# Kernel optimization log

Measured on AMD Instinct MI355X. Metric: run time of the kernel, lower is better.

## Reference

```python
import jax, jax.numpy as jnp
import numpy as np

D_IN = 1024
D_EMB = 512
HIDDEN = 256
NUM_CLASSES = 64
N_SUPPORT = 4096
N_QUERY = 8192


def setup_inputs() -> dict:
    key = jax.random.key(0)
    ks = jax.random.split(key, 8)
    scale_e = 1.0 / np.sqrt(D_IN)
    scale_1 = 1.0 / np.sqrt(2 * D_EMB)
    scale_2 = 1.0 / np.sqrt(HIDDEN)
    return {
        "support_data": jax.random.normal(ks[0], (N_SUPPORT, D_IN), jnp.float32),
        "query_data": jax.random.normal(ks[1], (N_QUERY, D_IN), jnp.float32),
        "support_label": jax.random.randint(ks[2], (N_SUPPORT,), 0, NUM_CLASSES, jnp.int32),
        "W_e": jax.random.normal(ks[3], (D_IN, D_EMB), jnp.float32) * scale_e,
        "b_e": jnp.zeros((D_EMB,), jnp.float32),
        "W1": jax.random.normal(ks[4], (2 * D_EMB, HIDDEN), jnp.float32) * scale_1,
        "b1": jnp.zeros((HIDDEN,), jnp.float32),
        "W2": jax.random.normal(ks[5], (HIDDEN, 1), jnp.float32) * scale_2,
        "b2": jnp.zeros((1,), jnp.float32),
    }


def reference(support_data, query_data, support_label, W_e, b_e, W1, b1, W2, b2):
    # embedding_net: Linear + ReLU
    s_emb = jax.nn.relu(support_data @ W_e + b_e)  # [Ns, D_EMB]
    q_emb = jax.nn.relu(query_data @ W_e + b_e)    # [Nq, D_EMB]

    # per-class mean of support embeddings (segment mean; labels are 0..C-1,
    # matching torch.unique()'s sorted order)
    sums = jax.ops.segment_sum(s_emb, support_label, num_segments=NUM_CLASSES)
    counts = jax.ops.segment_sum(jnp.ones((s_emb.shape[0],), s_emb.dtype),
                                 support_label, num_segments=NUM_CLASSES)
    means = sums / jnp.maximum(counts, 1.0)[:, None]  # [C, D_EMB]

    # relation_net on concat(query, class_mean): split first linear so the
    # [Nq*C, 2*D_EMB] concat is never materialized (same math).
    Wq, Wc = W1[:D_EMB], W1[D_EMB:]
    h = jax.nn.relu(q_emb @ Wq[:, None, :].squeeze(1) @ jnp.eye(HIDDEN, dtype=W1.dtype)
                    if False else
                    (q_emb @ Wq)[:, None, :] + (means @ Wc)[None, :, :] + b1)  # [Nq, C, HIDDEN]
    scores = jax.nn.sigmoid(h @ W2 + b2)  # [Nq, C, 1]
    # torch version stacks [1,1]-shaped scores -> [Nq, C, 1, 1]
    return scores[:, :, None, :]
```

## Files before the change

### kernel.cpp

```cpp
#include <hip/hip_runtime.h>
#include <hip/hip_bf16.h>

#define D_IN 1024
#define D_EMB 512
#define HIDDEN 256
#define NUM_CLASSES 64
#define N_SUPPORT 4096
#define N_QUERY 8192

typedef __bf16 bf16x8 __attribute__((ext_vector_type(8)));
typedef __bf16 bf16x4 __attribute__((ext_vector_type(4)));
typedef float f32x4 __attribute__((ext_vector_type(4)));

#define GLOAD_LDS16(g, l)                                                          \
  __builtin_amdgcn_global_load_lds(                                                \
      (const __attribute__((address_space(1))) unsigned int*)(g),                  \
      (__attribute__((address_space(3))) unsigned int*)(l), 16, 0, 0)

__global__ void transpose_weights(const float* __restrict__ W_e,
                                  const float* __restrict__ W1,
                                  __bf16* __restrict__ WeT,
                                  __bf16* __restrict__ WqT) {
  __shared__ float tile[32][33];
  const float* in;
  __bf16* out;
  int bx, by, rows, cols;
  int b = blockIdx.x;
  if (b < 512) {
    in = W_e; out = WeT; rows = D_IN; cols = D_EMB;
    bx = (b & 15) * 32; by = (b >> 4) * 32;
  } else {
    b -= 512;
    in = W1; out = WqT; rows = D_EMB; cols = HIDDEN;
    bx = (b & 7) * 32; by = (b >> 3) * 32;
  }
  int tx = threadIdx.x;
  int ty = threadIdx.y;
#pragma unroll
  for (int i = ty; i < 32; i += 8)
    tile[i][tx] = in[(long)(by + i) * cols + bx + tx];
  __syncthreads();
#pragma unroll
  for (int i = ty; i < 32; i += 8)
    out[(long)(bx + i) * rows + by + tx] = (__bf16)tile[tx][i];
}

__global__ __launch_bounds__(256, 2) void gemm_emb(
    const float* __restrict__ support, const float* __restrict__ query,
    const __bf16* __restrict__ BT, const float* __restrict__ bias,
    __bf16* __restrict__ C) {
  constexpr int BM = 128, BN = 128, BK = 32;
  constexpr int N = D_EMB, K = D_IN;
  constexpr int LDA_S = 40;
  constexpr int WN = BN / 2, NR = WN / 16, MR = 4;

  __shared__ __align__(16) __bf16 As[BM * LDA_S];
  __shared__ __align__(16) __bf16 Bs[BN * BK];

  const int tid = threadIdx.x;
  const int wave = tid >> 6;
  const int lane = tid & 63;
  const int m0 = blockIdx.x * BM;
  const int n0 = blockIdx.y * BN;
  const int wr = wave >> 1;
  const int wc = wave & 1;
  const int l16 = lane & 15;
  const int half = lane >> 4;

  const float* Abase =
      (m0 < N_SUPPORT) ? (support + (long)m0 * K) : (query + (long)(m0 - N_SUPPORT) * K);

  f32x4 acc[MR][NR];
#pragma unroll
  for (int m = 0; m < MR; ++m)
#pragma unroll
    for (int n = 0; n < NR; ++n) acc[m][n] = (f32x4)0.0f;

  for (int k0 = 0; k0 < K; k0 += BK) {
    float4 av[4];
#pragma unroll
    for (int q = 0; q < 4; ++q) {
      int idx = q * 256 + tid;
      int row = idx >> 3;
      int c4 = idx & 7;
      av[q] = *(const float4*)(Abase + (long)row * K + k0 + c4 * 4);
    }
#pragma unroll
    for (int q = 0; q < 2; ++q) {
      int chunk = q * 256 + tid;
      int row = chunk >> 2;
      int kc = chunk & 3;
      GLOAD_LDS16(BT + (long)(n0 + row) * K + k0 + kc * 8, Bs + chunk * 8);
    }
#pragma unroll
    for (int q = 0; q < 4; ++q) {
      int idx = q * 256 + tid;
      int row = idx >> 3;
      int c4 = idx & 7;
      bf16x4 o;
      o[0] = (__bf16)av[q].x; o[1] = (__bf16)av[q].y;
      o[2] = (__bf16)av[q].z; o[3] = (__bf16)av[q].w;
      *(bf16x4*)(As + row * LDA_S + c4 * 4) = o;
    }
    asm volatile("s_waitcnt vmcnt(0)" ::: "memory");
    __syncthreads();

    bf16x8 a[MR], b[NR];
#pragma unroll
    for (int m = 0; m < MR; ++m)
      a[m] = *(const bf16x8*)(As + (wr * 64 + m * 16 + l16) * LDA_S + half * 8);
#pragma unroll
    for (int n = 0; n < NR; ++n)
      b[n] = *(const bf16x8*)(Bs + (wc * WN + n * 16 + l16) * BK + half * 8);
#pragma unroll
    for (int m = 0; m < MR; ++m)
#pragma unroll
      for (int n = 0; n < NR; ++n)
        acc[m][n] = __builtin_amdgcn_mfma_f32_16x16x32_bf16(a[m], b[n],
                                                            acc[m][n], 0, 0, 0);
    __syncthreads();
  }

#pragma unroll
  for (int m = 0; m < MR; ++m)
#pragma unroll
    for (int n = 0; n < NR; ++n)
#pragma unroll
      for (int j = 0; j < 4; ++j) {
        int row = m0 + wr * 64 + m * 16 + half * 4 + j;
        int col = n0 + wc * WN + n * 16 + l16;
        float v = fmaxf(acc[m][n][j] + bias[col], 0.0f);
        C[(long)row * N + col] = (__bf16)v;
      }
}

__global__ __launch_bounds__(256, 2) void gemm_qp(
    const __bf16* __restrict__ A, const __bf16* __restrict__ BT,
    const float* __restrict__ bias, float* __restrict__ C, int M, int N, int K) {
  constexpr int BM = 128, BN = 64, BK = 32;
  constexpr int WN = BN / 2, NR = WN / 16, MR = 4;

  __shared__ __align__(16) __bf16 As[BM * BK];
  __shared__ __align__(16) __bf16 Bs[BN * BK];

  const int tid = threadIdx.x;
  const int wave = tid >> 6;
  const int lane = tid & 63;
  const int m0 = blockIdx.x * BM;
  const int n0 = blockIdx.y * BN;
  const int wr = wave >> 1;
  const int wc = wave & 1;
  const int l16 = lane & 15;
  const int half = lane >> 4;

  f32x4 acc[MR][NR];
#pragma unroll
  for (int m = 0; m < MR; ++m)
#pragma unroll
    for (int n = 0; n < NR; ++n) acc[m][n] = (f32x4)0.0f;

  for (int k0 = 0; k0 < K; k0 += BK) {
#pragma unroll
    for (int q = 0; q < BM / 64; ++q) {
      int chunk = q * 256 + tid;
      int row = chunk >> 2;
      int kc = chunk & 3;
      GLOAD_LDS16(A + (long)(m0 + row) * K + k0 + kc * 8, As + chunk * 8);
    }
    {
      int chunk = tid;
      int row = chunk >> 2;
      int kc = chunk & 3;
      GLOAD_LDS16(BT + (long)(n0 + row) * K + k0 + kc * 8, Bs + chunk * 8);
    }
    asm volatile("s_waitcnt vmcnt(0)" ::: "memory");
    __syncthreads();

    bf16x8 a[MR], b[NR];
#pragma unroll
    for (int m = 0; m < MR; ++m)
      a[m] = *(const bf16x8*)(As + (wr * 64 + m * 16 + l16) * BK + half * 8);
#pragma unroll
    for (int n = 0; n < NR; ++n)
      b[n] = *(const bf16x8*)(Bs + (wc * WN + n * 16 + l16) * BK + half * 8);
#pragma unroll
    for (int m = 0; m < MR; ++m)
#pragma unroll
      for (int n = 0; n < NR; ++n)
        acc[m][n] = __builtin_amdgcn_mfma_f32_16x16x32_bf16(a[m], b[n],
                                                            acc[m][n], 0, 0, 0);
    __syncthreads();
  }

#pragma unroll
  for (int m = 0; m < MR; ++m)
#pragma unroll
    for (int n = 0; n < NR; ++n)
#pragma unroll
      for (int j = 0; j < 4; ++j) {
        int row = m0 + wr * 64 + m * 16 + half * 4 + j;
        int col = n0 + wc * WN + n * 16 + l16;
        C[(long)row * N + col] = acc[m][n][j] + bias[col];
      }
}

__global__ __launch_bounds__(256) void proto_partial(
    const __bf16* __restrict__ s_emb, const int* __restrict__ labels,
    float* __restrict__ sums_part, int* __restrict__ cnt_part) {
  const int c = blockIdx.x;
  const int s = blockIdx.y;
  const int tid = threadIdx.x;
  const int j0 = s * (N_SUPPORT / 8);
  float a0 = 0.0f, a1 = 0.0f;
  int count = 0;
#pragma unroll 4
  for (int j = j0; j < j0 + N_SUPPORT / 8; j += 4) {
    int4 lab4 = *(const int4*)(labels + j);
#pragma unroll
    for (int u = 0; u < 4; ++u) {
      int lab = (u == 0) ? lab4.x : (u == 1) ? lab4.y : (u == 2) ? lab4.z : lab4.w;
      if (lab == c) {
        const __bf16* r = s_emb + (long)(j + u) * D_EMB;
        a0 += (float)r[tid];
        a1 += (float)r[tid + 256];
        ++count;
      }
    }
  }
  float* dst = sums_part + (long)(c * 8 + s) * D_EMB;
  dst[tid] = a0;
  dst[tid + 256] = a1;
  if (tid == 0) cnt_part[c * 8 + s] = count;
}

__global__ __launch_bounds__(256) void proto_cpb(
    const float* __restrict__ sums_part, const int* __restrict__ cnt_part,
    const float* __restrict__ W1, float* __restrict__ cpb_part) {
  __shared__ float ls[128];
  const int c = blockIdx.x;
  const int kc = blockIdx.y;
  const int k0 = kc * 128;
  const int tid = threadIdx.x;

  int nc = 0;
#pragma unroll
  for (int s = 0; s < 8; ++s) nc += cnt_part[c * 8 + s];
  float inv = 1.0f / fmaxf((float)nc, 1.0f);

  if (tid < 128) {
    float v = 0.0f;
#pragma unroll
    for (int s = 0; s < 8; ++s)
      v += sums_part[(long)(c * 8 + s) * D_EMB + k0 + tid];
    ls[tid] = v * inv;
  }
  __syncthreads();

  float acc = 0.0f;
#pragma unroll 8
  for (int k = 0; k < 128; ++k)
    acc = fmaf(ls[k], W1[(long)(D_EMB + k0 + k) * HIDDEN + tid], acc);
  cpb_part[((long)kc * NUM_CLASSES + c) * HIDDEN + tid] = acc;
}

__global__ void cpb_reduce(const float* __restrict__ cpb_part,
                           float* __restrict__ cpb) {
  int i = blockIdx.x * 256 + threadIdx.x;
  const int n = NUM_CLASSES * HIDDEN;
  cpb[i] = cpb_part[i] + cpb_part[n + i] + cpb_part[2 * n + i] +
           cpb_part[3 * n + i];
}

__global__ __launch_bounds__(256) void score_kernel(
    const float* __restrict__ qp, const float* __restrict__ cpb,
    const float* __restrict__ W2, const float* __restrict__ b2,
    float* __restrict__ out) {
  constexpr int CPB_S = 260;
  __shared__ __align__(16) float cpb_s[NUM_CLASSES * CPB_S];
  __shared__ __align__(16) float qp_s[32 * HIDDEN];
  __shared__ __align__(16) float w2_s[HIDDEN];

  const int tid = threadIdx.x;
  const int w = tid >> 6;
  const int c = tid & 63;
  const int qb0 = blockIdx.x * 32;

  w2_s[tid] = W2[tid];
  for (int i = tid; i < NUM_CLASSES * HIDDEN; i += 256)
    cpb_s[(i >> 8) * CPB_S + (i & (HIDDEN - 1))] = cpb[i];
  for (int i = tid; i < 32 * HIDDEN; i += 256)
    qp_s[i] = qp[(long)qb0 * HIDDEN + i];
  __syncthreads();

  const float bb = b2[0];
  float acc[8];
#pragma unroll
  for (int q = 0; q < 8; ++q) acc[q] = 0.0f;

  const float* crow = cpb_s + c * CPB_S;
  const float* qbase = qp_s + (w * 8) * HIDDEN;

#pragma unroll 4
  for (int kc = 0; kc < HIDDEN / 4; ++kc) {
    f32x4 cv = *(const f32x4*)(crow + kc * 4);
    f32x4 wv = *(const f32x4*)(w2_s + kc * 4);
#pragma unroll
    for (int q = 0; q < 8; ++q) {
      f32x4 qv = *(const f32x4*)(qbase + q * HIDDEN + kc * 4);
      acc[q] = fmaf(fmaxf(qv[0] + cv[0], 0.0f), wv[0], acc[q]);
      acc[q] = fmaf(fmaxf(qv[1] + cv[1], 0.0f), wv[1], acc[q]);
      acc[q] = fmaf(fmaxf(qv[2] + cv[2], 0.0f), wv[2], acc[q]);
      acc[q] = fmaf(fmaxf(qv[3] + cv[3], 0.0f), wv[3], acc[q]);
    }
  }

#pragma unroll
  for (int q = 0; q < 8; ++q) {
    float x = acc[q] + bb;
    out[(long)(qb0 + w * 8 + q) * NUM_CLASSES + c] = 1.0f / (1.0f + __expf(-x));
  }
}

extern "C" void kernel_launch(void* const* d_in, const int* in_sizes, int n_in,
                              void* d_out, int out_size, void* d_ws,
                              size_t ws_size, hipStream_t stream) {
  const float* support = (const float*)d_in[0];
  const float* query   = (const float*)d_in[1];
  const int*   labels  = (const int*)d_in[2];
  const float* W_e     = (const float*)d_in[3];
  const float* b_e     = (const float*)d_in[4];
  const float* W1      = (const float*)d_in[5];
  const float* b1      = (const float*)d_in[6];
  const float* W2      = (const float*)d_in[7];
  const float* b2      = (const float*)d_in[8];
  float* out = (float*)d_out;

  char* ws = (char*)d_ws;
  size_t off = 0;
  auto alloc = [&](size_t bytes) {
    void* p = ws + off;
    off = (off + bytes + 255) & ~(size_t)255;
    return p;
  };
  const long NTOT = N_SUPPORT + N_QUERY;
  __bf16* WeT = (__bf16*)alloc((size_t)D_EMB * D_IN * 2);
  __bf16* WqT = (__bf16*)alloc((size_t)HIDDEN * D_EMB * 2);
  __bf16* emb = (__bf16*)alloc((size_t)NTOT * D_EMB * 2);
  float*  qp  = (float*)alloc((size_t)N_QUERY * HIDDEN * 4);
  float*  sums_part = (float*)alloc((size_t)NUM_CLASSES * 8 * D_EMB * 4);
  int*    cnt_part  = (int*)alloc((size_t)NUM_CLASSES * 8 * 4);
  float*  cpb_part  = (float*)alloc((size_t)4 * NUM_CLASSES * HIDDEN * 4);
  float*  cpb       = (float*)alloc((size_t)NUM_CLASSES * HIDDEN * 4);

  transpose_weights<<<640, dim3(32, 8), 0, stream>>>(W_e, W1, WeT, WqT);

  gemm_emb<<<dim3(NTOT / 128, D_EMB / 128), 256, 0, stream>>>(
      support, query, WeT, b_e, emb);

  proto_partial<<<dim3(NUM_CLASSES, 8), 256, 0, stream>>>(emb, labels, sums_part,
                                                          cnt_part);
  proto_cpb<<<dim3(NUM_CLASSES, 4), 256, 0, stream>>>(sums_part, cnt_part, W1,
                                                      cpb_part);
  cpb_reduce<<<NUM_CLASSES * HIDDEN / 256, 256, 0, stream>>>(cpb_part, cpb);

  gemm_qp<<<dim3(N_QUERY / 128, HIDDEN / 64), 256, 0, stream>>>(
      emb + (long)N_SUPPORT * D_EMB, WqT, b1, qp, N_QUERY, HIDDEN, D_EMB);

  score_kernel<<<N_QUERY / 32, 256, 0, stream>>>(qp, cpb, W2, b2, out);
}
```

Baseline: 100.0 us.

## Double-buffer LDS in both GEMMs, shrink emb tile, add grouped block swizzle

Both GEMM kernels now use double-buffered shared memory, so the global loads for the next K-tile are issued before the MFMA work on the current tile and only one barrier is needed per iteration. gemm_emb shrinks its N tile from 128 to 64, which doubles the grid to 768 blocks. Both kernels switch to a 1D grid with a grouped mapping (8 M-tiles per group) to improve L2 reuse of the A rows. The costs are more LDS per block and higher register pressure from holding the A prefetch, and the smaller N tile means each fp32 A row is read and converted twice as often.

Result: no change. 101.1 us (+1.0%).

```diff
diff --git a/kernel.cpp b/kernel.cpp
--- a/kernel.cpp
+++ b/kernel.cpp
@@ -49,26 +49,34 @@
     const float* __restrict__ support, const float* __restrict__ query,
     const __bf16* __restrict__ BT, const float* __restrict__ bias,
     __bf16* __restrict__ C) {
-  constexpr int BM = 128, BN = 128, BK = 32;
+  constexpr int BM = 128, BN = 64, BK = 32;
   constexpr int N = D_EMB, K = D_IN;
   constexpr int LDA_S = 40;
-  constexpr int WN = BN / 2, NR = WN / 16, MR = 4;
-
-  __shared__ __align__(16) __bf16 As[BM * LDA_S];
-  __shared__ __align__(16) __bf16 Bs[BN * BK];
+  constexpr int NT = K / BK;
+  constexpr int MR = 4, NR = 2;
+
+  __shared__ __align__(16) __bf16 As[2][BM * LDA_S];
+  __shared__ __align__(16) __bf16 Bs[2][BN * BK];
 
   const int tid = threadIdx.x;
-  const int wave = tid >> 6;
-  const int lane = tid & 63;
-  const int m0 = blockIdx.x * BM;
-  const int n0 = blockIdx.y * BN;
-  const int wr = wave >> 1;
-  const int wc = wave & 1;
-  const int l16 = lane & 15;
-  const int half = lane >> 4;
-
-  const float* Abase =
-      (m0 < N_SUPPORT) ? (support + (long)m0 * K) : (query + (long)(m0 - N_SUPPORT) * K);
+  const int wave = tid >> 6, lane = tid & 63;
+  const int wr = wave >> 1, wc = wave & 1;
+  const int l16 = lane & 15, half = lane >> 4;
+
+  const int s = blockIdx.x;
+  const int m_t = (s & 7) + (s >> 6) * 8;
+  const int n_t = (s >> 3) & 7;
+  const int m0 = m_t * BM, n0 = n_t * BN;
+
+  const float* Abase = (m0 < N_SUPPORT)
+                           ? support + (long)m0 * K
+                           : query + (long)(m0 - N_SUPPORT) * K;
+
+  const int ar0 = tid >> 2, ar1 = (tid + 256) >> 2;
+  const int ac = tid & 3;
+  const int brow = tid >> 2, bkc = tid & 3;
+
+  float4 av[2][2];
 
   f32x4 acc[MR][NR];
 #pragma unroll
@@ -76,50 +84,70 @@
 #pragma unroll
     for (int n = 0; n < NR; ++n) acc[m][n] = (f32x4)0.0f;
 
-  for (int k0 = 0; k0 < K; k0 += BK) {
-    float4 av[4];
-#pragma unroll
-    for (int q = 0; q < 4; ++q) {
-      int idx = q * 256 + tid;
-      int row = idx >> 3;
-      int c4 = idx & 7;
-      av[q] = *(const float4*)(Abase + (long)row * K + k0 + c4 * 4);
-    }
-#pragma unroll
-    for (int q = 0; q < 2; ++q) {
-      int chunk = q * 256 + tid;
-      int row = chunk >> 2;
-      int kc = chunk & 3;
-      GLOAD_LDS16(BT + (long)(n0 + row) * K + k0 + kc * 8, Bs + chunk * 8);
-    }
-#pragma unroll
-    for (int q = 0; q < 4; ++q) {
-      int idx = q * 256 + tid;
-      int row = idx >> 3;
-      int c4 = idx & 7;
-      bf16x4 o;
-      o[0] = (__bf16)av[q].x; o[1] = (__bf16)av[q].y;
-      o[2] = (__bf16)av[q].z; o[3] = (__bf16)av[q].w;
-      *(bf16x4*)(As + row * LDA_S + c4 * 4) = o;
-    }
-    asm volatile("s_waitcnt vmcnt(0)" ::: "memory");
+#define LOAD_A(t)                                                         \
+  {                                                                       \
+    const float* p0 = Abase + (long)ar0 * K + (t) * BK + ac * 8;          \
+    const float* p1 = Abase + (long)ar1 * K + (t) * BK + ac * 8;          \
+    av[0][0] = *(const float4*)(p0);                                      \
+    av[0][1] = *(const float4*)(p0 + 4);                                  \
+    av[1][0] = *(const float4*)(p1);                                      \
+    av[1][1] = *(const float4*)(p1 + 4);                                  \
+  }
+
+#define WRITE_A(buf)                                                      \
+  {                                                                       \
+    bf16x8 o0, o1;                                                        \
+    o0[0] = (__bf16)av[0][0].x; o0[1] = (__bf16)av[0][0].y;               \
+    o0[2] = (__bf16)av[0][0].z; o0[3] = (__bf16)av[0][0].w;               \
+    o0[4] = (__bf16)av[0][1].x; o0[5] = (__bf16)av[0][1].y;               \
+    o0[6] = (__bf16)av[0][1].z; o0[7] = (__bf16)av[0][1].w;               \
+    o1[0] = (__bf16)av[1][0].x; o1[1] = (__bf16)av[1][0].y;               \
+    o1[2] = (__bf16)av[1][0].z; o1[3] = (__bf16)av[1][0].w;               \
+    o1[4] = (__bf16)av[1][1].x; o1[5] = (__bf16)av[1][1].y;               \
+    o1[6] = (__bf16)av[1][1].z; o1[7] = (__bf16)av[1][1].w;               \
+    *(bf16x8*)(&As[buf][ar0 * LDA_S + ac * 8]) = o0;                      \
+    *(bf16x8*)(&As[buf][ar1 * LDA_S + ac * 8]) = o1;                      \
+  }
+
+#define GLD_B(t, buf)                                                     \
+  GLOAD_LDS16(BT + (long)(n0 + brow) * K + (t) * BK + bkc * 8,            \
+              &Bs[buf][tid * 8]);
+
+#define COMPUTE(buf)                                                      \
+  {                                                                       \
+    bf16x8 a[MR], b[NR];                                                  \
+    _Pragma("unroll") for (int m = 0; m < MR; ++m)                        \
+        a[m] = *(const bf16x8*)(&As[buf][(wr * 64 + m * 16 + l16) *       \
+                                             LDA_S + half * 8]);          \
+    _Pragma("unroll") for (int n = 0; n < NR; ++n)                        \
+        b[n] = *(const bf16x8*)(&Bs[buf][(wc * 32 + n * 16 + l16) * BK +  \
+                                         half * 8]);                      \
+    _Pragma("unroll") for (int m = 0; m < MR; ++m)                        \
+        _Pragma("unroll") for (int n = 0; n < NR; ++n)                    \
+            acc[m][n] = __builtin_amdgcn_mfma_f32_16x16x32_bf16(          \
+                a[m], b[n], acc[m][n], 0, 0, 0);                          \
+  }
+
+  LOAD_A(0);
+  GLD_B(0, 0);
+  WRITE_A(0);
+  __syncthreads();
+
+  int cur = 0;
+  for (int t = 0; t < NT - 1; ++t) {
+    LOAD_A(t + 1);
+    GLD_B(t + 1, cur ^ 1);
+    COMPUTE(cur);
+    WRITE_A(cur ^ 1);
     __syncthreads();
-
-    bf16x8 a[MR], b[NR];
-#pragma unroll
-    for (int m = 0; m < MR; ++m)
-      a[m] = *(const bf16x8*)(As + (wr * 64 + m * 16 + l16) * LDA_S + half * 8);
-#pragma unroll
-    for (int n = 0; n < NR; ++n)
-      b[n] = *(const bf16x8*)(Bs + (wc * WN + n * 16 + l16) * BK + half * 8);
-#pragma unroll
-    for (int m = 0; m < MR; ++m)
-#pragma unroll
-      for (int n = 0; n < NR; ++n)
-        acc[m][n] = __builtin_amdgcn_mfma_f32_16x16x32_bf16(a[m], b[n],
-                                                            acc[m][n], 0, 0, 0);
-    __syncthreads();
-  }
+    cur ^= 1;
+  }
+  COMPUTE(cur);
+
+#undef LOAD_A
+#undef WRITE_A
+#undef GLD_B
+#undef COMPUTE
 
 #pragma unroll
   for (int m = 0; m < MR; ++m)
@@ -128,7 +156,7 @@
 #pragma unroll
       for (int j = 0; j < 4; ++j) {
         int row = m0 + wr * 64 + m * 16 + half * 4 + j;
-        int col = n0 + wc * WN + n * 16 + l16;
+        int col = n0 + wc * 32 + n * 16 + l16;
         float v = fmaxf(acc[m][n][j] + bias[col], 0.0f);
         C[(long)row * N + col] = (__bf16)v;
       }
@@ -136,22 +164,28 @@
 
 __global__ __launch_bounds__(256, 2) void gemm_qp(
     const __bf16* __restrict__ A, const __bf16* __restrict__ BT,
-    const float* __restrict__ bias, float* __restrict__ C, int M, int N, int K) {
+    const float* __restrict__ bias, float* __restrict__ C) {
   constexpr int BM = 128, BN = 64, BK = 32;
-  constexpr int WN = BN / 2, NR = WN / 16, MR = 4;
-
-  __shared__ __align__(16) __bf16 As[BM * BK];
-  __shared__ __align__(16) __bf16 Bs[BN * BK];
+  constexpr int N = HIDDEN, K = D_EMB;
+  constexpr int NT = K / BK;
+  constexpr int MR = 4, NR = 2;
+
+  __shared__ __align__(16) __bf16 As[2][BM * BK];
+  __shared__ __align__(16) __bf16 Bs[2][BN * BK];
 
   const int tid = threadIdx.x;
-  const int wave = tid >> 6;
-  const int lane = tid & 63;
-  const int m0 = blockIdx.x * BM;
-  const int n0 = blockIdx.y * BN;
-  const int wr = wave >> 1;
-  const int wc = wave & 1;
-  const int l16 = lane & 15;
-  const int half = lane >> 4;
+  const int wave = tid >> 6, lane = tid & 63;
+  const int wr = wave >> 1, wc = wave & 1;
+  const int l16 = lane & 15, half = lane >> 4;
+
+  const int s = blockIdx.x;
+  const int m_t = (s & 7) + (s >> 5) * 8;
+  const int n_t = (s >> 3) & 3;
+  const int m0 = m_t * BM, n0 = n_t * BN;
+
+  const int arow0 = tid >> 2, arow1 = (tid + 256) >> 2;
+  const int akc = tid & 3;
+  const int brow = tid >> 2, bkc = tid & 3;
 
   f32x4 acc[MR][NR];
 #pragma unroll
@@ -159,38 +193,45 @@
 #pragma unroll
     for (int n = 0; n < NR; ++n) acc[m][n] = (f32x4)0.0f;
 
-  for (int k0 = 0; k0 < K; k0 += BK) {
-#pragma unroll
-    for (int q = 0; q < BM / 64; ++q) {
-      int chunk = q * 256 + tid;
-      int row = chunk >> 2;
-      int kc = chunk & 3;
-      GLOAD_LDS16(A + (long)(m0 + row) * K + k0 + kc * 8, As + chunk * 8);
-    }
-    {
-      int chunk = tid;
-      int row = chunk >> 2;
-      int kc = chunk & 3;
-      GLOAD_LDS16(BT + (long)(n0 + row) * K + k0 + kc * 8, Bs + chunk * 8);
-    }
-    asm volatile("s_waitcnt vmcnt(0)" ::: "memory");
+#define STAGE(t, buf)                                                     \
+  {                                                                       \
+    GLOAD_LDS16(A + (long)(m0 + arow0) * K + (t) * BK + akc * 8,          \
+                &As[buf][tid * 8]);                                       \
+    GLOAD_LDS16(A + (long)(m0 + arow1) * K + (t) * BK + akc * 8,          \
+                &As[buf][(tid + 256) * 8]);                               \
+    GLOAD_LDS16(BT + (long)(n0 + brow) * K + (t) * BK + bkc * 8,          \
+                &Bs[buf][tid * 8]);                                       \
+  }
+
+#define COMPUTE(buf)                                                      \
+  {                                                                       \
+    bf16x8 a[MR], b[NR];                                                  \
+    _Pragma("unroll") for (int m = 0; m < MR; ++m)                        \
+        a[m] = *(const bf16x8*)(&As[buf][(wr * 64 + m * 16 + l16) * BK +  \
+                                         half * 8]);                      \
+    _Pragma("unroll") for (int n = 0; n < NR; ++n)                        \
+        b[n] = *(const bf16x8*)(&Bs[buf][(wc * 32 + n * 16 + l16) * BK +  \
+                                         half * 8]);                      \
+    _Pragma("unroll") for (int m = 0; m < MR; ++m)                        \
+        _Pragma("unroll") for (int n = 0; n < NR; ++n)                    \
+            acc[m][n] = __builtin_amdgcn_mfma_f32_16x16x32_bf16(          \
+                a[m], b[n], acc[m][n], 0, 0, 0);                          \
+  }
+
+  STAGE(0, 0);
+  __syncthreads();
+
+  int cur = 0;
+  for (int t = 0; t < NT - 1; ++t) {
+    STAGE(t + 1, cur ^ 1);
+    COMPUTE(cur);
     __syncthreads();
-
-    bf16x8 a[MR], b[NR];
-#pragma unroll
-    for (int m = 0; m < MR; ++m)
-      a[m] = *(const bf16x8*)(As + (wr * 64 + m * 16 + l16) * BK + half * 8);
-#pragma unroll
-    for (int n = 0; n < NR; ++n)
-      b[n] = *(const bf16x8*)(Bs + (wc * WN + n * 16 + l16) * BK + half * 8);
-#pragma unroll
-    for (int m = 0; m < MR; ++m)
-#pragma unroll
-      for (int n = 0; n < NR; ++n)
-        acc[m][n] = __builtin_amdgcn_mfma_f32_16x16x32_bf16(a[m], b[n],
-                                                            acc[m][n], 0, 0, 0);
-    __syncthreads();
-  }
+    cur ^= 1;
+  }
+  COMPUTE(cur);
+
+#undef STAGE
+#undef COMPUTE
 
 #pragma unroll
   for (int m = 0; m < MR; ++m)
@@ -199,7 +240,7 @@
 #pragma unroll
       for (int j = 0; j < 4; ++j) {
         int row = m0 + wr * 64 + m * 16 + half * 4 + j;
-        int col = n0 + wc * WN + n * 16 + l16;
+        int col = n0 + wc * 32 + n * 16 + l16;
         C[(long)row * N + col] = acc[m][n][j] + bias[col];
       }
 }
@@ -354,8 +395,7 @@
 
   transpose_weights<<<640, dim3(32, 8), 0, stream>>>(W_e, W1, WeT, WqT);
 
-  gemm_emb<<<dim3(NTOT / 128, D_EMB / 128), 256, 0, stream>>>(
-      support, query, WeT, b_e, emb);
+  gemm_emb<<<768, 256, 0, stream>>>(support, query, WeT, b_e, emb);
 
   proto_partial<<<dim3(NUM_CLASSES, 8), 256, 0, stream>>>(emb, labels, sums_part,
                                                           cnt_part);
@@ -363,8 +403,7 @@
                                                       cpb_part);
   cpb_reduce<<<NUM_CLASSES * HIDDEN / 256, 256, 0, stream>>>(cpb_part, cpb);
 
-  gemm_qp<<<dim3(N_QUERY / 128, HIDDEN / 64), 256, 0, stream>>>(
-      emb + (long)N_SUPPORT * D_EMB, WqT, b1, qp, N_QUERY, HIDDEN, D_EMB);
+  gemm_qp<<<256, 256, 0, stream>>>(emb + (long)N_SUPPORT * D_EMB, WqT, b1, qp);
 
   score_kernel<<<N_QUERY / 32, 256, 0, stream>>>(qp, cpb, W2, b2, out);
 }
```

## Replace LDS-tiled GEMMs with single-wave register-only GEMM template

Applied to the files above, without the earlier changes.

Both GEMMs (embedding and query projection) are replaced with one templated kernel in which a single 64-thread wave computes a 64x64 tile. The wave loads A and B fragments straight from global memory into registers, with no LDS staging and no barriers. This removes the shared-memory round trip and the __syncthreads overhead. In exchange, operands are no longer shared across waves, so global and L2 traffic rises, and the fragment loads are strided and less coalesced.

Result: slower. 141.7 us (+41.6%).

```diff
diff --git a/kernel.cpp b/kernel.cpp
--- a/kernel.cpp
+++ b/kernel.cpp
@@ -9,13 +9,7 @@
 #define N_QUERY 8192
 
 typedef __bf16 bf16x8 __attribute__((ext_vector_type(8)));
-typedef __bf16 bf16x4 __attribute__((ext_vector_type(4)));
 typedef float f32x4 __attribute__((ext_vector_type(4)));
-
-#define GLOAD_LDS16(g, l)                                                          \
-  __builtin_amdgcn_global_load_lds(                                                \
-      (const __attribute__((address_space(1))) unsigned int*)(g),                  \
-      (__attribute__((address_space(3))) unsigned int*)(l), 16, 0, 0)
 
 __global__ void transpose_weights(const float* __restrict__ W_e,
                                   const float* __restrict__ W1,
@@ -45,162 +39,89 @@
     out[(long)(bx + i) * rows + by + tx] = (__bf16)tile[tx][i];
 }
 
-__global__ __launch_bounds__(256, 2) void gemm_emb(
-    const float* __restrict__ support, const float* __restrict__ query,
-    const __bf16* __restrict__ BT, const float* __restrict__ bias,
-    __bf16* __restrict__ C) {
-  constexpr int BM = 128, BN = 128, BK = 32;
-  constexpr int N = D_EMB, K = D_IN;
-  constexpr int LDA_S = 40;
-  constexpr int WN = BN / 2, NR = WN / 16, MR = 4;
-
-  __shared__ __align__(16) __bf16 As[BM * LDA_S];
-  __shared__ __align__(16) __bf16 Bs[BN * BK];
-
-  const int tid = threadIdx.x;
-  const int wave = tid >> 6;
-  const int lane = tid & 63;
-  const int m0 = blockIdx.x * BM;
-  const int n0 = blockIdx.y * BN;
-  const int wr = wave >> 1;
-  const int wc = wave & 1;
+template <int K, bool A_FP32, bool OUT_BF16>
+__global__ __launch_bounds__(64) void gemm_nolds(
+    const float* __restrict__ Asup, const float* __restrict__ Aqry,
+    const __bf16* __restrict__ Abf, const __bf16* __restrict__ BT,
+    const float* __restrict__ bias, void* __restrict__ Cv, int Ncols) {
+  const int lane = threadIdx.x;
   const int l16 = lane & 15;
   const int half = lane >> 4;
-
-  const float* Abase =
-      (m0 < N_SUPPORT) ? (support + (long)m0 * K) : (query + (long)(m0 - N_SUPPORT) * K);
-
-  f32x4 acc[MR][NR];
-#pragma unroll
-  for (int m = 0; m < MR; ++m)
-#pragma unroll
-    for (int n = 0; n < NR; ++n) acc[m][n] = (f32x4)0.0f;
-
-  for (int k0 = 0; k0 < K; k0 += BK) {
-    float4 av[4];
-#pragma unroll
-    for (int q = 0; q < 4; ++q) {
-      int idx = q * 256 + tid;
-      int row = idx >> 3;
-      int c4 = idx & 7;
-      av[q] = *(const float4*)(Abase + (long)row * K + k0 + c4 * 4);
+  const int m0 = blockIdx.x * 64;
+  const int n0 = blockIdx.y * 64;
+
+  const float* Af = nullptr;
+  const __bf16* Ab = nullptr;
+  if (A_FP32) {
+    Af = (m0 < N_SUPPORT) ? Asup + (long)m0 * K
+                          : Aqry + (long)(m0 - N_SUPPORT) * K;
+  } else {
+    Ab = Abf + (long)m0 * K;
+  }
+
+  int arow[4], brow[4];
+#pragma unroll
+  for (int m = 0; m < 4; ++m) arow[m] = (m * 16 + l16) * K;
+#pragma unroll
+  for (int n = 0; n < 4; ++n) brow[n] = (n0 + n * 16 + l16) * K;
+
+  f32x4 acc[4][4];
+#pragma unroll
+  for (int m = 0; m < 4; ++m)
+#pragma unroll
+    for (int n = 0; n < 4; ++n) acc[m][n] = (f32x4)0.0f;
+
+#pragma unroll 2
+  for (int s = 0; s < K / 32; ++s) {
+    const int kb = s * 32 + half * 8;
+    bf16x8 a[4], b[4];
+#pragma unroll
+    for (int n = 0; n < 4; ++n)
+      b[n] = *(const bf16x8*)(BT + brow[n] + kb);
+    if (A_FP32) {
+#pragma unroll
+      for (int m = 0; m < 4; ++m) {
+        f32x4 lo = *(const f32x4*)(Af + arow[m] + kb);
+        f32x4 hi = *(const f32x4*)(Af + arow[m] + kb + 4);
+        bf16x8 t;
+        t[0] = (__bf16)lo[0]; t[1] = (__bf16)lo[1];
+        t[2] = (__bf16)lo[2]; t[3] = (__bf16)lo[3];
+        t[4] = (__bf16)hi[0]; t[5] = (__bf16)hi[1];
+        t[6] = (__bf16)hi[2]; t[7] = (__bf16)hi[3];
+        a[m] = t;
+      }
+    } else {
+#pragma unroll
+      for (int m = 0; m < 4; ++m)
+        a[m] = *(const bf16x8*)(Ab + arow[m] + kb);
     }
 #pragma unroll
-    for (int q = 0; q < 2; ++q) {
-      int chunk = q * 256 + tid;
-      int row = chunk >> 2;
-      int kc = chunk & 3;
-      GLOAD_LDS16(BT + (long)(n0 + row) * K + k0 + kc * 8, Bs + chunk * 8);
-    }
-#pragma unroll
-    for (int q = 0; q < 4; ++q) {
-      int idx = q * 256 + tid;
-      int row = idx >> 3;
-      int c4 = idx & 7;
-      bf16x4 o;
-      o[0] = (__bf16)av[q].x; o[1] = (__bf16)av[q].y;
-      o[2] = (__bf16)av[q].z; o[3] = (__bf16)av[q].w;
-      *(bf16x4*)(As + row * LDA_S + c4 * 4) = o;
-    }
-    asm volatile("s_waitcnt vmcnt(0)" ::: "memory");
-    __syncthreads();
-
-    bf16x8 a[MR], b[NR];
-#pragma unroll
-    for (int m = 0; m < MR; ++m)
-      a[m] = *(const bf16x8*)(As + (wr * 64 + m * 16 + l16) * LDA_S + half * 8);
-#pragma unroll
-    for (int n = 0; n < NR; ++n)
-      b[n] = *(const bf16x8*)(Bs + (wc * WN + n * 16 + l16) * BK + half * 8);
-#pragma unroll
-    for (int m = 0; m < MR; ++m)
-#pragma unroll
-      for (int n = 0; n < NR; ++n)
+    for (int m = 0; m < 4; ++m)
+#pragma unroll
+      for (int n = 0; n < 4; ++n)
         acc[m][n] = __builtin_amdgcn_mfma_f32_16x16x32_bf16(a[m], b[n],
                                                             acc[m][n], 0, 0, 0);
-    __syncthreads();
-  }
-
-#pragma unroll
-  for (int m = 0; m < MR; ++m)
-#pragma unroll
-    for (int n = 0; n < NR; ++n)
+  }
+
+  float bs[4];
+#pragma unroll
+  for (int n = 0; n < 4; ++n) bs[n] = bias[n0 + n * 16 + l16];
+
+#pragma unroll
+  for (int m = 0; m < 4; ++m)
+#pragma unroll
+    for (int n = 0; n < 4; ++n)
 #pragma unroll
       for (int j = 0; j < 4; ++j) {
-        int row = m0 + wr * 64 + m * 16 + half * 4 + j;
-        int col = n0 + wc * WN + n * 16 + l16;
-        float v = fmaxf(acc[m][n][j] + bias[col], 0.0f);
-        C[(long)row * N + col] = (__bf16)v;
-      }
-}
-
-__global__ __launch_bounds__(256, 2) void gemm_qp(
-    const __bf16* __restrict__ A, const __bf16* __restrict__ BT,
-    const float* __restrict__ bias, float* __restrict__ C, int M, int N, int K) {
-  constexpr int BM = 128, BN = 64, BK = 32;
-  constexpr int WN = BN / 2, NR = WN / 16, MR = 4;
-
-  __shared__ __align__(16) __bf16 As[BM * BK];
-  __shared__ __align__(16) __bf16 Bs[BN * BK];
-
-  const int tid = threadIdx.x;
-  const int wave = tid >> 6;
-  const int lane = tid & 63;
-  const int m0 = blockIdx.x * BM;
-  const int n0 = blockIdx.y * BN;
-  const int wr = wave >> 1;
-  const int wc = wave & 1;
-  const int l16 = lane & 15;
-  const int half = lane >> 4;
-
-  f32x4 acc[MR][NR];
-#pragma unroll
-  for (int m = 0; m < MR; ++m)
-#pragma unroll
-    for (int n = 0; n < NR; ++n) acc[m][n] = (f32x4)0.0f;
-
-  for (int k0 = 0; k0 < K; k0 += BK) {
-#pragma unroll
-    for (int q = 0; q < BM / 64; ++q) {
-      int chunk = q * 256 + tid;
-      int row = chunk >> 2;
-      int kc = chunk & 3;
-      GLOAD_LDS16(A + (long)(m0 + row) * K + k0 + kc * 8, As + chunk * 8);
-    }
-    {
-      int chunk = tid;
-      int row = chunk >> 2;
-      int kc = chunk & 3;
-      GLOAD_LDS16(BT + (long)(n0 + row) * K + k0 + kc * 8, Bs + chunk * 8);
-    }
-    asm volatile("s_waitcnt vmcnt(0)" ::: "memory");
-    __syncthreads();
-
-    bf16x8 a[MR], b[NR];
-#pragma unroll
-    for (int m = 0; m < MR; ++m)
-      a[m] = *(const bf16x8*)(As + (wr * 64 + m * 16 + l16) * BK + half * 8);
-#pragma unroll
-    for (int n = 0; n < NR; ++n)
-      b[n] = *(const bf16x8*)(Bs + (wc * WN + n * 16 + l16) * BK + half * 8);
-#pragma unroll
-    for (int m = 0; m < MR; ++m)
-#pragma unroll
-      for (int n = 0; n < NR; ++n)
-        acc[m][n] = __builtin_amdgcn_mfma_f32_16x16x32_bf16(a[m], b[n],
-                                                            acc[m][n], 0, 0, 0);
-    __syncthreads();
-  }
-
-#pragma unroll
-  for (int m = 0; m < MR; ++m)
-#pragma unroll
-    for (int n = 0; n < NR; ++n)
-#pragma unroll
-      for (int j = 0; j < 4; ++j) {
-        int row = m0 + wr * 64 + m * 16 + half * 4 + j;
-        int col = n0 + wc * WN + n * 16 + l16;
-        C[(long)row * N + col] = acc[m][n][j] + bias[col];
+        int row = m0 + m * 16 + half * 4 + j;
+        int col = n0 + n * 16 + l16;
+        float v = acc[m][n][j] + bs[n];
+        if (OUT_BF16) {
+          v = fmaxf(v, 0.0f);
+          ((__bf16*)Cv)[(long)row * Ncols + col] = (__bf16)v;
+        } else {
+          ((float*)Cv)[(long)row * Ncols + col] = v;
+        }
       }
 }
 
@@ -354,8 +275,9 @@
 
   transpose_weights<<<640, dim3(32, 8), 0, stream>>>(W_e, W1, WeT, WqT);
 
-  gemm_emb<<<dim3(NTOT / 128, D_EMB / 128), 256, 0, stream>>>(
-      support, query, WeT, b_e, emb);
+  gemm_nolds<D_IN, true, true>
+      <<<dim3(NTOT / 64, D_EMB / 64), 64, 0, stream>>>(
+          support, query, nullptr, WeT, b_e, emb, D_EMB);
 
   proto_partial<<<dim3(NUM_CLASSES, 8), 256, 0, stream>>>(emb, labels, sums_part,
                                                           cnt_part);
@@ -363,8 +285,9 @@
                                                       cpb_part);
   cpb_reduce<<<NUM_CLASSES * HIDDEN / 256, 256, 0, stream>>>(cpb_part, cpb);
 
-  gemm_qp<<<dim3(N_QUERY / 128, HIDDEN / 64), 256, 0, stream>>>(
-      emb + (long)N_SUPPORT * D_EMB, WqT, b1, qp, N_QUERY, HIDDEN, D_EMB);
+  gemm_nolds<D_EMB, false, false>
+      <<<dim3(N_QUERY / 64, HIDDEN / 64), 64, 0, stream>>>(
+          nullptr, nullptr, emb + (long)N_SUPPORT * D_EMB, WqT, b1, qp, HIDDEN);
 
   score_kernel<<<N_QUERY / 32, 256, 0, stream>>>(qp, cpb, W2, b2, out);
 }
```
